# Performance work log

Hardware: AMD Instinct MI355X
Metric: run time of the kernel (lower is better)

Reference implementation:

```python
import jax, jax.numpy as jnp
import numpy as np

S, B, T, H, E, V, OOV = 400, 16, 64, 512, 256, 50000, 50


def _w(k, shape, scale=0.02):
    return scale * jax.random.normal(k, shape, dtype=jnp.float32)


def setup_inputs() -> dict:
    key = jax.random.key(0)
    ks = jax.random.split(key, 20)
    H2 = H // 2
    return {
        "inputs": jax.random.randint(ks[0], (S, B), 0, V),
        "inputs_length": jnp.full((B,), S, dtype=jnp.int32),  # full lengths (packing is then a no-op)
        "inputs_extended": jax.random.randint(ks[1], (S, B), 0, V + OOV),
        "oov_size": OOV,
        "outputs": jax.random.randint(ks[2], (T, B), 0, V),
        "embedding": _w(ks[3], (V, E)),
        "enc_Wih_f": _w(ks[4], (4 * H2, E)), "enc_Whh_f": _w(ks[5], (4 * H2, H2)),
        "enc_bih_f": jnp.zeros(4 * H2), "enc_bhh_f": jnp.zeros(4 * H2),
        "enc_Wih_b": _w(ks[6], (4 * H2, E)), "enc_Whh_b": _w(ks[7], (4 * H2, H2)),
        "enc_bih_b": jnp.zeros(4 * H2), "enc_bhh_b": jnp.zeros(4 * H2),
        "feat_W": _w(ks[8], (H, H)),
        "dec_Wih": _w(ks[9], (4 * H, E)), "dec_Whh": _w(ks[10], (4 * H, H)),
        "dec_bih": jnp.zeros(4 * H), "dec_bhh": jnp.zeros(4 * H),
        "attn_W": _w(ks[11], (H, H)),
        "vocab_W": _w(ks[12], (V, 3 * H)), "vocab_b": jnp.zeros(V),
        "ptr_W": _w(ks[13], (1, 3 * H)), "ptr_b": jnp.zeros(1),
    }


def _lstm(xs, Wih, Whh, bih, bhh, reverse=False):
    # xs: [S, B, E] -> ys [S, B, H2], final (h, c)
    Bn, H2 = xs.shape[1], Whh.shape[1]

    def step(carry, x):
        h, c = carry
        g = x @ Wih.T + bih + h @ Whh.T + bhh
        i, f, gg, o = jnp.split(g, 4, axis=-1)  # pytorch gate order i,f,g,o
        c = jax.nn.sigmoid(f) * c + jax.nn.sigmoid(i) * jnp.tanh(gg)
        h = jax.nn.sigmoid(o) * jnp.tanh(c)
        return (h, c), h

    init = (jnp.zeros((Bn, H2), xs.dtype), jnp.zeros((Bn, H2), xs.dtype))
    (h, c), ys = jax.lax.scan(step, init, xs, reverse=reverse)
    return ys, h, c


def _forward(inputs, inputs_extended, oov_size, outputs, embedding,
             enc_Wih_f, enc_Whh_f, enc_bih_f, enc_bhh_f,
             enc_Wih_b, enc_Whh_b, enc_bih_b, enc_bhh_b,
             feat_W, dec_Wih, dec_Whh, dec_bih, dec_bhh,
             attn_W, vocab_W, vocab_b, ptr_W, ptr_b):
    Hn = dec_Whh.shape[1]
    Tn, Bn = outputs.shape
    Sn = inputs.shape[0]

    x = embedding[inputs]  # [S,B,E]
    yf, hf, cf = _lstm(x, enc_Wih_f, enc_Whh_f, enc_bih_f, enc_bhh_f)
    yb, hb, cb = _lstm(x, enc_Wih_b, enc_Whh_b, enc_bih_b, enc_bhh_b, reverse=True)
    enc_seq = jnp.concatenate([yf, yb], axis=-1)              # [S,B,H]
    enc_out = jnp.transpose(enc_seq @ feat_W.T, (1, 2, 0))    # Permute(1,2,0) -> [B,H,S]
    # View(-1, H) on [2,B,H/2] stacked states (faithful reshape, incl. batch mixing)
    h0 = jnp.stack([hf, hb]).reshape(-1, Hn)                  # [B,H]
    c0 = jnp.stack([cf, cb]).reshape(-1, Hn)

    yemb = embedding[outputs]                                 # [T,B,E]
    idx = inputs_extended.T                                   # [B,S]
    rows = jnp.arange(Bn)[:, None]
    t_ids = jnp.arange(Tn)

    def step(carry, inp):
        t, xt = inp
        h, c, prev_attn, hid_buf = carry
        # LSTMCell
        g = xt @ dec_Wih.T + dec_bih + h @ dec_Whh.T + dec_bhh
        i, f, gg, o = jnp.split(g, 4, axis=-1)
        c = jax.nn.sigmoid(f) * c + jax.nn.sigmoid(i) * jnp.tanh(gg)
        h = jax.nn.sigmoid(o) * jnp.tanh(c)
        # intra-temporal attention (NB: faithful to source, the *normalized*
        # previous attention is fed back as temporal_scores_sum)
        scores = jnp.exp(jnp.einsum('bh,bhs->bs', h, enc_out))   # [B,S]
        attn = jnp.where(t == 0, scores, scores / prev_attn)
        attn = attn / attn.sum(-1, keepdims=True)                # Normalize(-1)
        enc_ctx = jnp.einsum('bs,bhs->bh', attn, enc_out)        # [B,H]
        # intra-decoder attention over previous decoder hiddens
        keys = hid_buf @ attn_W.T                                # [T,B,H]
        sc = jnp.einsum('bh,tbh->bt', h, keys)
        sc = jnp.where(t_ids[None, :] < t, sc, -1e30)
        a = jax.nn.softmax(sc, axis=-1)
        dec_ctx = jnp.where(t == 0, 0.0, jnp.einsum('bt,tbh->bh', a, hid_buf))
        hid_buf = hid_buf.at[t].set(h)
        # pointer-generator
        feats = jnp.concatenate([h, enc_ctx, dec_ctx], axis=-1)  # [B,3H]
        vdist = jax.nn.softmax(feats @ vocab_W.T + vocab_b, axis=1)
        p = jax.nn.sigmoid(feats @ ptr_W.T + ptr_b)              # [B,1]
        vdist = (1.0 - p) * vdist
        copy = p * attn                                          # [B,S]
        vpad = jnp.pad(vdist, ((0, 0), (0, oov_size)))
        final = vpad.at[rows, idx].add(copy)                     # scatter_add
        return (h, c, attn, hid_buf), final

    hid_buf0 = jnp.zeros((Tn, Bn, Hn))
    init = (h0, c0, jnp.ones((Bn, Sn)), hid_buf0)
    _, preds = jax.lax.scan(step, init, (t_ids, yemb))
    return preds  # [T, B, V+oov]


def reference(inputs, inputs_length, inputs_extended, oov_size, outputs, embedding,
              enc_Wih_f, enc_Whh_f, enc_bih_f, enc_bhh_f,
              enc_Wih_b, enc_Whh_b, enc_bih_b, enc_bhh_b,
              feat_W, dec_Wih, dec_Whh, dec_bih, dec_bhh,
              attn_W, vocab_W, vocab_b, ptr_W, ptr_b):
    # inputs_length is full-length here, so packed RNN == plain scan
    return _forward(inputs, inputs_extended, oov_size, outputs, embedding,
                    enc_Wih_f, enc_Whh_f, enc_bih_f, enc_bhh_f,
                    enc_Wih_b, enc_Whh_b, enc_bih_b, enc_bhh_b,
                    feat_W, dec_Wih, dec_Whh, dec_bih, dec_bhh,
                    attn_W, vocab_W, vocab_b, ptr_W, ptr_b)
```

## Files before the change

### kernel.cpp

```cpp
#include <hip/hip_runtime.h>
#include <cstdint>
#include <cstddef>

typedef unsigned char uchar;
typedef unsigned short ushort;
typedef unsigned int uint;
typedef unsigned long long u64;
typedef __attribute__((ext_vector_type(4))) float f32x4;
typedef __attribute__((ext_vector_type(4))) uint u32x4;
typedef __attribute__((ext_vector_type(4))) int i32x4;

#define DI __device__ __forceinline__

#define S_  400
#define B_  16
#define T_  64
#define H_  512
#define H2_ 256
#define E_  256
#define V_  50000
#define VO_ 50050
#define LP_ 50048

constexpr size_t O_WENCWIH  = 0;
constexpr size_t O_WDECWIH  = O_WENCWIH + (size_t)2048*256*2;
constexpr size_t O_WDECWHH  = O_WDECWIH + (size_t)2048*256*2;
constexpr size_t O_WFEAT    = O_WDECWHH + (size_t)2048*512*2;
constexpr size_t O_WATTN    = O_WFEAT   + (size_t)512*512*2;
constexpr size_t O_BENC     = O_WATTN   + (size_t)512*512*2;
constexpr size_t O_BDEC     = O_BENC    + 2048*4;
constexpr size_t O_WENCWHH8 = O_BDEC    + 2048*4;
constexpr size_t O_XENC     = O_WENCWHH8+ (size_t)2*1024*256;
constexpr size_t O_XDEC     = O_XENC    + (size_t)6400*256*2;
constexpr size_t O_XINENC   = O_XDEC    + (size_t)1024*256*2;
constexpr size_t O_XD       = O_XINENC  + (size_t)2*400*16*1024*2;
constexpr size_t O_ENCSEQ   = O_XD      + (size_t)64*16*2048*2;
constexpr size_t O_ENCOUT   = O_ENCSEQ  + (size_t)6400*512*2;
constexpr size_t O_HFIN     = O_ENCOUT  + (size_t)16*400*512*2;
constexpr size_t O_CFIN     = O_HFIN    + 8192*4;
constexpr size_t O_HBUF     = O_CFIN    + 8192*4;
constexpr size_t O_CSTATE   = O_HBUF    + (size_t)2*8192*2;
constexpr size_t O_HIDBUF   = O_CSTATE  + 8192*4;
constexpr size_t O_KEYS     = O_HIDBUF  + (size_t)64*8192*2;
constexpr size_t O_ATTN     = O_KEYS    + (size_t)64*8192*2;
constexpr size_t O_ATTNQ    = O_ATTN    + (size_t)64*16*400*4;
constexpr size_t O_PSUM     = O_ATTNQ   + (size_t)64*16*400*4;
constexpr size_t O_CTXSLOT  = O_PSUM    + 2*32*16*4;
constexpr size_t O_FEATS    = O_CTXSLOT + (size_t)32*16*512*4;
constexpr size_t O_P        = O_FEATS   + (size_t)1024*1536;
constexpr size_t O_INVSUM   = O_P       + 1024*4;
constexpr size_t O_VOCAB8   = O_INVSUM  + 1024*4;
constexpr size_t O_LOGITS   = O_VOCAB8  + (size_t)50048*1536;
constexpr size_t O_A16      = O_XINENC;
constexpr size_t O_ENCT     = O_A16   + (size_t)16*64*416*2;
constexpr size_t O_HIDT     = O_ENCT  + (size_t)16*512*416*2;

DI float b2f(ushort u){ uint x = ((uint)u) << 16; return __builtin_bit_cast(float, x); }
DI ushort f2b(float f){
  uint u = __builtin_bit_cast(uint, f);
  return (ushort)((u + 0x7fffu + ((u >> 16) & 1u)) >> 16);
}
DI uchar f2e4(float f){
  int q = __builtin_amdgcn_cvt_pk_fp8_f32(f, 0.f, 0, false);
  return (uchar)(q & 0xff);
}
DI uchar f2i8(float f, float scale){
  float q = rintf(f * scale);
  q = fminf(127.f, fmaxf(-127.f, q));
  return (uchar)(signed char)(int)q;
}
DI float e42f(uint b){ return __builtin_amdgcn_cvt_f32_fp8((int)b, 0); }
DI float sigm(float x){ return 1.f / (1.f + __expf(-x)); }
DI float tanhf_(float x){ return 2.f / (1.f + __expf(-2.f * x)) - 1.f; }

DI f32x4 mfma16_bf16(u32x4 a, u32x4 b, f32x4 c){
  asm("v_mfma_f32_16x16x32_bf16 %0, %1, %2, %0" : "+v"(c) : "v"(a), "v"(b));
  return c;
}
DI f32x4 mfma16_fp8(u64 a, u64 b, f32x4 c){
  asm("v_mfma_f32_16x16x32_fp8_fp8 %0, %1, %2, %0" : "+v"(c) : "v"(a), "v"(b));
  return c;
}
DI i32x4 mfma16_i8(u32x4 a, u32x4 b, i32x4 c){
  asm("v_mfma_i32_16x16x64_i8 %0, %1, %2, %0" : "+v"(c) : "v"(a), "v"(b));
  return c;
}
DI void mfma_fence(){ asm volatile("s_nop 7\n\ts_nop 7"); }
DI void barrier_lds(){ asm volatile("s_waitcnt lgkmcnt(0)\n\ts_barrier" ::: "memory"); }
DI void wait_vm0(){ asm volatile("s_waitcnt vmcnt(0)" ::: "memory"); }

typedef __attribute__((address_space(1))) const uchar GU;
typedef __attribute__((address_space(3))) uchar LU;
DI void gload16(const uchar* g, uchar* l){
  __builtin_amdgcn_global_load_lds((GU*)g, (LU*)l, 16, 0, 0);
}

DI float fp8exp4(uint w){
  return __expf(__builtin_amdgcn_cvt_f32_fp8((int)w, 0) * (1.f/1024.f))
       + __expf(__builtin_amdgcn_cvt_f32_fp8((int)w, 1) * (1.f/1024.f))
       + __expf(__builtin_amdgcn_cvt_f32_fp8((int)w, 2) * (1.f/1024.f))
       + __expf(__builtin_amdgcn_cvt_f32_fp8((int)w, 3) * (1.f/1024.f));
}

struct X4 { ushort a, b, c, d; };

__global__ void k_prep(const float* __restrict__ eWf, const float* __restrict__ eWb,
                       const float* __restrict__ dW,  const float* __restrict__ dWhh,
                       const float* __restrict__ fW,  const float* __restrict__ aW,
                       const float* __restrict__ eHf, const float* __restrict__ eHb,
                       const float* __restrict__ bif, const float* __restrict__ bhf,
                       const float* __restrict__ bib, const float* __restrict__ bhb,
                       const float* __restrict__ dbi, const float* __restrict__ dbh,
                       ushort* __restrict__ oEW, ushort* __restrict__ oDW,
                       ushort* __restrict__ oDWhh, ushort* __restrict__ oF,
                       ushort* __restrict__ oA, uchar* __restrict__ oH8,
                       float* __restrict__ oBE, float* __restrict__ oBD){
  const int seg = blockIdx.y;
  const int stride = gridDim.x * 256;
  int n = 262144;
  if (seg == 2) n = 524288;
  else if (seg == 3) n = 1048576;
  else if (seg == 8 || seg == 9) n = 1024;
  else if (seg == 10) n = 2048;
  for (int i = blockIdx.x*256 + threadIdx.x; i < n; i += stride) {
    switch (seg) {
      case 0:  oEW[i]        = f2b(eWf[i]); break;
      case 1:  oEW[262144+i] = f2b(eWb[i]); break;
      case 2:  oDW[i]        = f2b(dW[i]);  break;
      case 3:  oDWhh[i]      = f2b(dWhh[i]);break;
      case 4:  oF[i]         = f2b(fW[i]);  break;
      case 5:  oA[i]         = f2b(aW[i]);  break;
      case 6:  oH8[i]        = f2i8(eHf[i], 1024.f); break;
      case 7:  oH8[262144+i] = f2i8(eHb[i], 1024.f); break;
      case 8:  oBE[i]        = bif[i]+bhf[i]; break;
      case 9:  oBE[1024+i]   = bib[i]+bhb[i]; break;
      case 10: oBD[i]        = dbi[i]+dbh[i]; break;
    }
  }
}

__global__ void k_embed(const int* __restrict__ inp, const int* __restrict__ outp,
                        const float* __restrict__ emb,
                        ushort* __restrict__ xenc, ushort* __restrict__ xdec){
  const int total1 = 6400*32, total2 = 1024*32;
  for (int i = blockIdx.x*256 + threadIdx.x; i < total1 + total2; i += gridDim.x*256) {
    const bool enc = i < total1;
    const int jj = enc ? i : i - total1;
    const int row = jj >> 5, e0 = (jj & 31) << 3;
    const int idx = enc ? inp[row] : outp[row];
    const float4* s4 = (const float4*)(emb + ((size_t)idx << 8) + e0);
    float4 v0 = s4[0], v1 = s4[1];
    uint4 o;
    o.x = (uint)f2b(v0.x) | ((uint)f2b(v0.y) << 16);
    o.y = (uint)f2b(v0.z) | ((uint)f2b(v0.w) << 16);
    o.z = (uint)f2b(v1.x) | ((uint)f2b(v1.y) << 16);
    o.w = (uint)f2b(v1.z) | ((uint)f2b(v1.w) << 16);
    *(uint4*)((enc ? xenc : xdec) + ((size_t)row << 8) + e0) = o;
  }
}

template<int ELSZ, int EPI>
__global__ __launch_bounds__(256)
void k_gemm(const uchar* __restrict__ A, const uchar* __restrict__ Bm,
            int mtiles, int kbytes, int arow, int brow,
            uchar* __restrict__ dst, const float* __restrict__ bias){
  __shared__ __align__(16) uchar sm[32768];
  const int tid = threadIdx.x;
  int bx = blockIdx.x;
  if ((gridDim.x & 7) == 0) {
    const int nb = gridDim.x >> 3;
    bx = (bx & 7) * nb + (bx >> 3);
  }
  const int mt = bx % mtiles, nt = bx / mtiles;
  const int m0 = mt << 7, n0 = nt << 7;
  const int w = tid >> 6, l = tid & 63, lr = l & 15, lh = l >> 4;
  const int wr = w >> 1, wc = w & 1;

  f32x4 acc[4][4];
#pragma unroll
  for (int i = 0; i < 4; ++i)
#pragma unroll
    for (int j = 0; j < 4; ++j) { f32x4 z = {0.f,0.f,0.f,0.f}; acc[i][j] = z; }

  const int iters = kbytes >> 6;
  const int roff = tid << 4;
  const int r0 = roff >> 6, c0 = roff & 63;
  const uchar* pa0 = A  + (size_t)(m0 + r0)      * arow + c0;
  const uchar* pa1 = A  + (size_t)(m0 + r0 + 64) * arow + c0;
  const uchar* pb0 = Bm + (size_t)(n0 + r0)      * brow + c0;
  const uchar* pb1 = Bm + (size_t)(n0 + r0 + 64) * brow + c0;

  auto issue = [&](int kt){
    const int ko = kt << 6;
    uchar* db = sm + ((kt & 1) << 14);
    gload16(pa0 + ko, db + roff);
    gload16(pa1 + ko, db + 4096 + roff);
    gload16(pb0 + ko, db + 8192 + roff);
    gload16(pb1 + ko, db + 12288 + roff);
  };

  issue(0);
  wait_vm0();
  __syncthreads();

  for (int kt = 0; kt < iters; ++kt) {
    if (kt + 1 < iters) issue(kt + 1);
    const uchar* smc = sm + ((kt & 1) << 14);
    if constexpr (ELSZ == 2) {
      u32x4 af[4], bf[4];
#pragma unroll
      for (int i = 0; i < 4; ++i) af[i] = *(const u32x4*)(smc + ((wr<<6)+(i<<4)+lr)*64 + (lh<<4));
#pragma unroll
      for (int j = 0; j < 4; ++j) bf[j] = *(const u32x4*)(smc + 8192 + ((wc<<6)+(j<<4)+lr)*64 + (lh<<4));
#pragma unroll
      for (int i = 0; i < 4; ++i)
#pragma unroll
        for (int j = 0; j < 4; ++j) acc[i][j] = mfma16_bf16(af[i], bf[j], acc[i][j]);
    } else {
#pragma unroll
      for (int kk = 0; kk < 2; ++kk) {
        u64 af[4], bf[4];
#pragma unroll
        for (int i = 0; i < 4; ++i) af[i] = *(const u64*)(smc + ((wr<<6)+(i<<4)+lr)*64 + (kk<<5) + (lh<<3));
#pragma unroll
        for (int j = 0; j < 4; ++j) bf[j] = *(const u64*)(smc + 8192 + ((wc<<6)+(j<<4)+lr)*64 + (kk<<5) + (lh<<3));
#pragma unroll
        for (int i = 0; i < 4; ++i)
#pragma unroll
          for (int j = 0; j < 4; ++j) acc[i][j] = mfma16_fp8(af[i], bf[j], acc[i][j]);
      }
    }
    wait_vm0();
    __syncthreads();
  }
  mfma_fence();

  if constexpr (EPI == 0 || EPI == 1) {
#pragma unroll
    for (int j = 0; j < 4; ++j) {
      const int n = n0 + (wc<<6) + (j<<4) + lr;
      const float bz = bias[n];
#pragma unroll
      for (int i = 0; i < 4; ++i)
#pragma unroll
        for (int r = 0; r < 4; ++r) {
          const int m = m0 + (wr<<6) + (i<<4) + (lh<<2) + r;
          const float v = acc[i][j][r] + bz;
          size_t addr;
          if constexpr (EPI == 0) {
            addr = ((size_t)((n >> 10)*6400 + m) << 10) + (n & 1023);
          } else {
            addr = ((size_t)m << 11) + n;
          }
          ((ushort*)dst)[addr] = f2b(v);
        }
    }
  } else if constexpr (EPI == 4) {
#pragma unroll
    for (int j = 0; j < 4; ++j) {
      const int n = n0 + (wc<<6) + (j<<4) + lr;
#pragma unroll
      for (int i = 0; i < 4; ++i)
#pragma unroll
        for (int r = 0; r < 4; ++r) {
          const int m = m0 + (wr<<6)+(i<<4)+(lh<<2)+r;
          ((ushort*)dst)[ ((size_t)m << 9) + n ] = f2b(acc[i][j][r]);
        }
    }
  } else {
    __syncthreads();
#pragma unroll
    for (int j = 0; j < 4; ++j) {
      const int nl = (wc<<6) + (j<<4) + lr;
      const int n = n0 + nl;
      const float bz = (n < V_) ? bias[n] : 0.f;
#pragma unroll
      for (int i = 0; i < 4; ++i)
#pragma unroll
        for (int r = 0; r < 4; ++r) {
          const int ml = (wr<<6)+(i<<4)+(lh<<2)+r;
          const float v = acc[i][j][r] * (1.f/2048.f) + bz;
          sm[ml*128 + nl] = f2e4(v * 1024.f);
        }
    }
    __syncthreads();
    const int row = tid >> 1, half = tid & 1;
    const uchar* srow = sm + row*128 + (half<<6);
    uchar* grow = dst + (size_t)(m0 + row) * LP_ + n0 + (half<<6);
#pragma unroll
    for (int cc4 = 0; cc4 < 4; ++cc4) {
      const int n = n0 + (half<<6) + (cc4<<4);
      if (n + 16 <= V_) {
        *(uint4*)(grow + (cc4<<4)) = *(const uint4*)(srow + (cc4<<4));
      } else {
        for (int bb = 0; bb < 16; ++bb) if (n + bb < V_) grow[(cc4<<4)+bb] = srow[(cc4<<4)+bb];
      }
    }
  }
}

__global__ __launch_bounds__(256)
void k_tr(const ushort* __restrict__ enc, ushort* __restrict__ encT){
  const int bid = blockIdx.x;
  const int b = bid / 20, rem = bid % 20;
  const int sc = rem >> 2, hc = rem & 3;
  const int s0 = sc*80, h0 = hc << 7;
  __shared__ ushort tl[80*130];
  const int t = threadIdx.x;
#pragma unroll
  for (int i = 0; i < 40; ++i) {
    const int idx = t + i*256;
    const int hh = idx & 127, si = idx >> 7;
    tl[si*130 + hh] = enc[ ((size_t)(((s0+si)<<4) + b) << 9) + h0 + hh ];
  }
  __syncthreads();
#pragma unroll
  for (int i = 0; i < 40; ++i) {
    const int idx = t + i*256;
    const int ss = idx % 80, hh = idx / 80;
    encT[ ((size_t)((b<<9) + h0 + hh))*416 + s0 + ss ] = tl[ss*130 + hh];
  }
}

__global__ __launch_bounds__(1024)
void k_encoder(const ushort* __restrict__ Xin, const uchar* __restrict__ Whh8,
               ushort* __restrict__ encseq, float* __restrict__ hfin, float* __restrict__ cfin,
               const float* __restrict__ vocabW, uchar* __restrict__ vocab8){
  const int bid = blockIdx.x;
  const int tid = threadIdx.x;
  if (bid >= 32) {
    const int n4 = 19200000, ntot4 = 19218432;
    const int stride = (gridDim.x - 32) * 1024;
    for (int i = (bid - 32)*1024 + tid; i < ntot4; i += stride) {
      uint o = 0;
      if (i < n4) {
        const float4 v = *(const float4*)(vocabW + (size_t)i*4);
        int lo = __builtin_amdgcn_cvt_pk_fp8_f32(v.x*16.f, v.y*16.f, 0, false);
        int hi = __builtin_amdgcn_cvt_pk_fp8_f32(v.z*16.f, v.w*16.f, 0, false);
        o = ((uint)lo & 0xffffu) | ((uint)hi << 16);
      }
      *(uint*)(vocab8 + (size_t)i*4) = o;
    }
    return;
  }
  const int d = bid >> 4, bglob = bid & 15;
  const int w = tid >> 6, l = tid & 63, lr = l & 15, lh = l >> 4;
  __shared__ __align__(16) uchar hl[2][1024];
  __shared__ float gl[1024];
  for (int i = tid; i < 2048; i += 1024) ((uchar*)hl)[i] = 0;
  u32x4 bfrag[4][4];
  const uchar* Wd = Whh8 + ((size_t)d << 18);
#pragma unroll
  for (int g = 0; g < 4; ++g)
#pragma unroll
    for (int kk = 0; kk < 4; ++kk)
      bfrag[g][kk] = *(const u32x4*)(Wd + (((size_t)((g<<8) + (w<<4) + lr)) << 8) + (kk<<6) + (lh<<4));
  const int base_a = (lr == 0) ? (lh << 4) : 512;
  const int astep  = (lr == 0) ? 64 : 0;
  const int u = tid;
  float cc = 0.f;
  const ushort* xin_base = Xin + ((size_t)(d*6400) << 10);

  auto xld = [&](int s) -> X4 {
    const int t = d ? 399 - s : s;
    const ushort* p = xin_base + (((size_t)(t*16 + bglob)) << 10) + u;
    X4 r; r.a = p[0]; r.b = p[256]; r.c = p[512]; r.d = p[768];
    return r;
  };

  auto STEP = [&](int s, X4 xv) {
    const int cur = s & 1;
    i32x4 z = {0,0,0,0};
    i32x4 a0 = z, a1 = z, a2 = z, a3 = z;
#pragma unroll
    for (int kk = 0; kk < 4; ++kk) {
      const u32x4 a = *(const u32x4*)&hl[cur][base_a + kk*astep];
      a0 = mfma16_i8(a, bfrag[0][kk], a0);
      a1 = mfma16_i8(a, bfrag[1][kk], a1);
      a2 = mfma16_i8(a, bfrag[2][kk], a2);
      a3 = mfma16_i8(a, bfrag[3][kk], a3);
    }
    mfma_fence();
    if (lh == 0) {
      const int uu = (w<<4) + lr;
      gl[uu]       = (float)a0[0];
      gl[256+uu]   = (float)a1[0];
      gl[512+uu]   = (float)a2[0];
      gl[768+uu]   = (float)a3[0];
    }
    barrier_lds();
    if (tid < 256) {
      const int t = d ? 399 - s : s;
      const float gi = b2f(xv.a) + gl[u]      *(1.f/8388608.f);
      const float gf = b2f(xv.b) + gl[256+u]  *(1.f/8388608.f);
      const float gg = b2f(xv.c) + gl[512+u]  *(1.f/8388608.f);
      const float go = b2f(xv.d) + gl[768+u]  *(1.f/8388608.f);
      cc = sigm(gf)*cc + sigm(gi)*tanhf_(gg);
      const float h = sigm(go)*tanhf_(cc);
      encseq[ ((size_t)((t<<4) + bglob) << 9) + (d<<8) + u ] = f2b(h);
      hl[cur^1][u] = f2i8(h, 8192.f);
      if (s == 399) {
        hfin[ (((d<<4)+bglob) << 8) + u ] = h;
        cfin[ (((d<<4)+bglob) << 8) + u ] = cc;
      }
    }
    barrier_lds();
  };

  X4 xv0 = {0,0,0,0};
  if (tid < 256) xv0 = xld(0);
  barrier_lds();
  for (int s = 0; s < 400; s += 2) {
    X4 xv1 = {0,0,0,0};
    if (tid < 256) xv1 = xld(s + 1);
    STEP(s, xv0);
    if (tid < 256) xv0 = xld(s + 2 <= 399 ? s + 2 : 399);
    STEP(s + 1, xv1);
  }
}

__global__ void k_h0z(const float* __restrict__ hfin, const float* __restrict__ cfin,
                      ushort* __restrict__ hbuf, float* __restrict__ cstate,
                      ushort* __restrict__ encT){
  const int tid = blockIdx.x*256 + threadIdx.x;
  if (tid < 8192) {
    const int r = tid >> 9, ch = tid & 511;
    const int d = r >> 3, b = ((r & 7) << 1) + (ch >> 8), u = ch & 255;
    const int src = (((d<<4)+b) << 8) + u;
    hbuf[8192 + tid] = f2b(hfin[src]);
    cstate[tid] = cfin[src];
  }
  if (tid < 16*512*16) {
    const int b = tid >> 13, h = (tid >> 4) & 511, sp = tid & 15;
    encT[((size_t)((b<<9) + h))*416 + 400 + sp] = 0;
  }
}

__global__ __launch_bounds__(256)
void k_lstm(int t, const ushort* __restrict__ Xd, const ushort* __restrict__ Whh,
            ushort* __restrict__ hbuf, float* __restrict__ cstate,
            ushort* __restrict__ hidbuf, ushort* __restrict__ hidT,
            uchar* __restrict__ feats){
  const int q = blockIdx.x, tid = threadIdx.x;
  const int w = tid >> 6, l = tid & 63, lr = l & 15, lh = l >> 4;
  __shared__ float gl[4][16][16];
  const ushort* hprev = hbuf + (((t+1)&1) << 13);
  f32x4 acc = {0.f,0.f,0.f,0.f};
  const ushort* Wrow = Whh + ((size_t)((w<<9) + (q<<4) + lr) << 9);
#pragma unroll
  for (int kk = 0; kk < 16; ++kk) {
    u32x4 a = *(const u32x4*)(hprev + (lr<<9) + (kk<<5) + (lh<<3));
    u32x4 b = *(const u32x4*)(Wrow + (kk<<5) + (lh<<3));
    acc = mfma16_bf16(a, b, acc);
  }
  mfma_fence();
#pragma unroll
  for (int r = 0; r < 4; ++r) {
    const int b = (lh<<2) + r;
    const float xvv = b2f(Xd[ ((size_t)((t<<4)+b) << 11) + (w<<9) + (q<<4) + lr ]);
    gl[w][b][lr] = acc[r] + xvv;
  }
  __syncthreads();
  const int b = tid >> 4, ul = tid & 15, uu = (q<<4) + ul;
  const float gi = gl[0][b][ul], gf = gl[1][b][ul], gg = gl[2][b][ul], go = gl[3][b][ul];
  float cc = cstate[(b<<9) + uu];
  cc = sigm(gf)*cc + sigm(gi)*tanhf_(gg);
  const float h = sigm(go)*tanhf_(cc);
  cstate[(b<<9)+uu] = cc;
  const ushort hb16 = f2b(h);
  hbuf[((t&1)<<13) + (b<<9) + uu] = hb16;
  hidbuf[((size_t)t<<13) + (b<<9) + uu] = hb16;
  hidT[((size_t)((b<<9)+uu) << 6) + t] = hb16;
  feats[(size_t)((t<<4)+b)*1536 + uu] = f2e4(h*128.f);
}

__global__ __launch_bounds__(256)
void k_score(const ushort* __restrict__ hid, const ushort* __restrict__ enc,
             float* __restrict__ E){
  const int b = blockIdx.x / 5, nc = blockIdx.x % 5;
  const int w = threadIdx.x >> 6, l = threadIdx.x & 63, lr = l & 15, lh = l >> 4;
  f32x4 acc[5];
#pragma unroll
  for (int j = 0; j < 5; ++j) { f32x4 z = {0.f,0.f,0.f,0.f}; acc[j] = z; }
#pragma unroll 4
  for (int kk = 0; kk < 16; ++kk) {
    const u32x4 a = *(const u32x4*)(hid + ((size_t)(((w<<4)+lr)<<4 | b) << 9) + (kk<<5) + (lh<<3));
#pragma unroll
    for (int j = 0; j < 5; ++j) {
      const int s = nc*80 + j*16 + lr;
      const u32x4 bb = *(const u32x4*)(enc + ((size_t)((s<<4) + b) << 9) + (kk<<5) + (lh<<3));
      acc[j] = mfma16_bf16(a, bb, acc[j]);
    }
  }
  mfma_fence();
#pragma unroll
  for (int j = 0; j < 5; ++j)
#pragma unroll
    for (int r = 0; r < 4; ++r) {
      const int t = (w<<4) + (lh<<2) + r;
      const int s = nc*80 + j*16 + lr;
      E[ ((size_t)(t*16 + b))*400 + s ] = __expf(acc[j][r]);
    }
}

__global__ __launch_bounds__(256)
void k_tnorm(const float* __restrict__ E, float* __restrict__ attnB,
             ushort* __restrict__ a16){
  const int b = blockIdx.x, tid = threadIdx.x;
  const int s0 = tid, s1 = tid + 256;
  __shared__ float red[4];
  __shared__ float bcv, qsv;
  float qp0 = 1.f, qp1 = 1.f, qsp = 1.f;
  for (int t = 0; t < 64; ++t) {
    const float e0 = E[ ((size_t)(t*16 + b))*400 + s0 ];
    const float e1 = (s1 < 400) ? E[ ((size_t)(t*16 + b))*400 + s1 ] : 0.f;
    const float q0 = t ? e0 * qsp / qp0 : e0;
    const float q1 = (s1 < 400) ? (t ? e1 * qsp / qp1 : e1) : 0.f;
    qp0 = q0; if (s1 < 400) qp1 = q1;
    float ss = q0 + q1;
#pragma unroll
    for (int off = 32; off > 0; off >>= 1) ss += __shfl_down(ss, off, 64);
    if ((tid & 63) == 0) red[tid >> 6] = ss;
    __syncthreads();
    if (tid == 0) {
      const float tot = red[0] + red[1] + red[2] + red[3];
      qsv = tot; bcv = 1.f / tot;
    }
    __syncthreads();
    const float inv = bcv;
    attnB[ ((size_t)(t*16 + b))*400 + s0 ] = q0 * inv;
    a16[ ((size_t)(b*64 + t))*416 + s0 ] = f2b(q0 * inv);
    if (s1 < 416) {
      if (s1 < 400) attnB[ ((size_t)(t*16 + b))*400 + s1 ] = q1 * inv;
      a16[ ((size_t)(b*64 + t))*416 + s1 ] = (s1 < 400) ? f2b(q1 * inv) : (ushort)0;
    }
    qsp = qsv;
    __syncthreads();
  }
}

__global__ __launch_bounds__(256)
void k_ctx(const ushort* __restrict__ a16, const ushort* __restrict__ encT,
           uchar* __restrict__ feats){
  const int b = blockIdx.x;
  const int w = threadIdx.x >> 6, l = threadIdx.x & 63, lr = l & 15, lh = l >> 4;
  f32x4 acc[4][8];
#pragma unroll
  for (int i = 0; i < 4; ++i)
#pragma unroll
    for (int j = 0; j < 8; ++j) { f32x4 z = {0.f,0.f,0.f,0.f}; acc[i][j] = z; }
  for (int kk = 0; kk < 13; ++kk) {
    u32x4 a[4];
#pragma unroll
    for (int mf = 0; mf < 4; ++mf)
      a[mf] = *(const u32x4*)(a16 + ((size_t)(b*64 + (mf<<4)+lr))*416 + (kk<<5) + (lh<<3));
#pragma unroll
    for (int j = 0; j < 8; ++j) {
      const int h = ((w<<3)+j)*16 + lr;
      const u32x4 bb = *(const u32x4*)(encT + ((size_t)((b<<9)+h))*416 + (kk<<5) + (lh<<3));
#pragma unroll
      for (int mf = 0; mf < 4; ++mf) acc[mf][j] = mfma16_bf16(a[mf], bb, acc[mf][j]);
    }
  }
  mfma_fence();
#pragma unroll
  for (int mf = 0; mf < 4; ++mf)
#pragma unroll
    for (int j = 0; j < 8; ++j)
#pragma unroll
      for (int r = 0; r < 4; ++r) {
        const int t = (mf<<4) + (lh<<2) + r;
        const int h = ((w<<3)+j)*16 + lr;
        feats[ (size_t)((t<<4)+b)*1536 + 512 + h ] = f2e4(acc[mf][j][r] * 128.f);
      }
}

__global__ __launch_bounds__(256)
void k_dattn(const ushort* __restrict__ hid, const ushort* __restrict__ keys,
             const ushort* __restrict__ hidT, uchar* __restrict__ feats){
  const int b = blockIdx.x;
  const int tid = threadIdx.x;
  const int w = tid >> 6, l = tid & 63, lr = l & 15, lh = l >> 4;
  __shared__ float sc[64*65];
  __shared__ ushort pb[64*72];
  {
    f32x4 acc[4];
#pragma unroll
    for (int i = 0; i < 4; ++i) { f32x4 z = {0.f,0.f,0.f,0.f}; acc[i] = z; }
#pragma unroll 4
    for (int kk = 0; kk < 16; ++kk) {
      const u32x4 bb = *(const u32x4*)(keys + ((size_t)((((w<<4)+lr)<<4) + b) << 9) + (kk<<5) + (lh<<3));
#pragma unroll
      for (int mf = 0; mf < 4; ++mf) {
        const u32x4 a = *(const u32x4*)(hid + ((size_t)((((mf<<4)+lr)<<4) + b) << 9) + (kk<<5) + (lh<<3));
        acc[mf] = mfma16_bf16(a, bb, acc[mf]);
      }
    }
    mfma_fence();
#pragma unroll
    for (int mf = 0; mf < 4; ++mf)
#pragma unroll
      for (int r = 0; r < 4; ++r)
        sc[ ((mf<<4)+(lh<<2)+r)*65 + (w<<4)+lr ] = acc[mf][r];
  }
  __syncthreads();
  for (int rr = 0; rr < 16; ++rr) {
    const int row = (w<<4) + rr;
    const float v = sc[row*65 + l];
    const bool act = l < row;
    float vm = act ? v : -3.0e38f;
    float m = vm;
#pragma unroll
    for (int off = 32; off > 0; off >>= 1) m = fmaxf(m, __shfl_xor(m, off, 64));
    const float e = act ? __expf(vm - m) : 0.f;
    float ssum = e;
#pragma unroll
    for (int off = 32; off > 0; off >>= 1) ssum += __shfl_xor(ssum, off, 64);
    const float p = (row == 0) ? 0.f : e / ssum;
    pb[row*72 + l] = f2b(p);
  }
  __syncthreads();
  {
    f32x4 acc[4][8];
#pragma unroll
    for (int i = 0; i < 4; ++i)
#pragma unroll
      for (int j = 0; j < 8; ++j) { f32x4 z = {0.f,0.f,0.f,0.f}; acc[i][j] = z; }
#pragma unroll
    for (int kk = 0; kk < 2; ++kk) {
      u32x4 a[4];
#pragma unroll
      for (int mf = 0; mf < 4; ++mf)
        a[mf] = *(const u32x4*)&pb[ ((mf<<4)+lr)*72 + (kk<<5) + (lh<<3) ];
#pragma unroll
      for (int j = 0; j < 8; ++j) {
        const int h = ((w<<3)+j)*16 + lr;
        const u32x4 bb = *(const u32x4*)(hidT + ((size_t)((b<<9)+h) << 6) + (kk<<5) + (lh<<3));
#pragma unroll
        for (int mf = 0; mf < 4; ++mf) acc[mf][j] = mfma16_bf16(a[mf], bb, acc[mf][j]);
      }
    }
    mfma_fence();
#pragma unroll
    for (int mf = 0; mf < 4; ++mf)
#pragma unroll
      for (int j = 0; j < 8; ++j)
#pragma unroll
        for (int r = 0; r < 4; ++r) {
          const int t = (mf<<4) + (lh<<2) + r;
          const int h = ((w<<3)+j)*16 + lr;
          feats[ (size_t)((t<<4)+b)*1536 + 1024 + h ] = f2e4(acc[mf][j][r] * 128.f);
        }
  }
}

__global__ __launch_bounds__(256)
void k_final2(const uchar* __restrict__ logits, const uchar* __restrict__ feats,
              const float* __restrict__ ptrW, const float* __restrict__ ptrb,
              const float* __restrict__ attnB, const int* __restrict__ iext,
              float* __restrict__ out){
  const int row = blockIdx.x, tid = threadIdx.x;
  const uchar* lrow = logits + (size_t)row * LP_;
  float s = 0.f;
  for (int c = tid*16; c < V_; c += 4096) {
    const uint4 v = *(const uint4*)(lrow + c);
    s += fp8exp4(v.x) + fp8exp4(v.y) + fp8exp4(v.z) + fp8exp4(v.w);
  }
  const uchar* f = feats + (size_t)row*1536;
  float pd = 0.f;
  for (int k = tid*4; k < 1536; k += 1024) {
    const uint wv = *(const uint*)(f + k);
    pd += __builtin_amdgcn_cvt_f32_fp8((int)wv,0)*ptrW[k]
        + __builtin_amdgcn_cvt_f32_fp8((int)wv,1)*ptrW[k+1]
        + __builtin_amdgcn_cvt_f32_fp8((int)wv,2)*ptrW[k+2]
        + __builtin_amdgcn_cvt_f32_fp8((int)wv,3)*ptrW[k+3];
  }
#pragma unroll
  for (int off = 32; off > 0; off >>= 1) {
    s  += __shfl_down(s,  off, 64);
    pd += __shfl_down(pd, off, 64);
  }
  __shared__ float wsum[4], wpd[4];
  __shared__ float oms, pvs;
  if ((tid & 63) == 0) { wsum[tid>>6] = s; wpd[tid>>6] = pd; }
  __syncthreads();
  if (tid == 0) {
    const float pv = sigm((wpd[0]+wpd[1]+wpd[2]+wpd[3]) * (1.f/128.f) + ptrb[0]);
    pvs = pv;
    oms = (1.f - pv) / (wsum[0]+wsum[1]+wsum[2]+wsum[3]);
  }
  __syncthreads();
  const float om = oms;
  float* orow = out + (size_t)row * VO_;
  for (int v = tid; v < VO_; v += 256) {
    float val = 0.f;
    if (v < V_) val = om * __expf(e42f((uint)lrow[v]) * (1.f/1024.f));
    orow[v] = val;
  }
  __syncthreads();
  const float pv = pvs;
  const int b = row & 15;
  const float* arow = attnB + (size_t)row*400;
  for (int sidx = tid; sidx < 400; sidx += 256) {
    atomicAdd(orow + iext[sidx*16 + b], pv * arow[sidx]);
  }
}

extern "C" void kernel_launch(void* const* d_in, const int* in_sizes, int n_in,
                              void* d_out, int out_size, void* d_ws, size_t ws_size,
                              hipStream_t stream){
  (void)in_sizes; (void)n_in; (void)out_size; (void)ws_size;
  const int*   inputs     = (const int*)  d_in[0];
  const int*   inputs_ext = (const int*)  d_in[2];
  const int*   outputs    = (const int*)  d_in[4];
  const float* embedding  = (const float*)d_in[5];
  const float* enc_Wih_f  = (const float*)d_in[6];
  const float* enc_Whh_f  = (const float*)d_in[7];
  const float* enc_bih_f  = (const float*)d_in[8];
  const float* enc_bhh_f  = (const float*)d_in[9];
  const float* enc_Wih_b  = (const float*)d_in[10];
  const float* enc_Whh_b  = (const float*)d_in[11];
  const float* enc_bih_b  = (const float*)d_in[12];
  const float* enc_bhh_b  = (const float*)d_in[13];
  const float* feat_W     = (const float*)d_in[14];
  const float* dec_Wih    = (const float*)d_in[15];
  const float* dec_Whh    = (const float*)d_in[16];
  const float* dec_bih    = (const float*)d_in[17];
  const float* dec_bhh    = (const float*)d_in[18];
  const float* attn_W     = (const float*)d_in[19];
  const float* vocab_W    = (const float*)d_in[20];
  const float* vocab_b    = (const float*)d_in[21];
  const float* ptr_W      = (const float*)d_in[22];
  const float* ptr_b      = (const float*)d_in[23];

  uchar* W = (uchar*)d_ws;
  ushort* wEncWih  = (ushort*)(W + O_WENCWIH);
  ushort* wDecWih  = (ushort*)(W + O_WDECWIH);
  ushort* wDecWhh  = (ushort*)(W + O_WDECWHH);
  ushort* wFeat    = (ushort*)(W + O_WFEAT);
  ushort* wAttn    = (ushort*)(W + O_WATTN);
  float*  bEnc     = (float*) (W + O_BENC);
  float*  bDec     = (float*) (W + O_BDEC);
  uchar*  wEncWhh8 = (uchar*) (W + O_WENCWHH8);
  ushort* xEnc     = (ushort*)(W + O_XENC);
  ushort* xDec     = (ushort*)(W + O_XDEC);
  ushort* XinEnc   = (ushort*)(W + O_XINENC);
  ushort* Xd       = (ushort*)(W + O_XD);
  ushort* encSeq   = (ushort*)(W + O_ENCSEQ);
  ushort* encOut   = (ushort*)(W + O_ENCOUT);
  float*  hFin     = (float*) (W + O_HFIN);
  float*  cFin     = (float*) (W + O_CFIN);
  ushort* hBuf     = (ushort*)(W + O_HBUF);
  float*  cState   = (float*) (W + O_CSTATE);
  ushort* hidBuf   = (ushort*)(W + O_HIDBUF);
  ushort* keys     = (ushort*)(W + O_KEYS);
  float*  attnB    = (float*) (W + O_ATTN);
  float*  Ebuf     = (float*) (W + O_ATTNQ);
  ushort* a16      = (ushort*)(W + O_A16);
  ushort* encT     = (ushort*)(W + O_ENCT);
  ushort* hidT     = (ushort*)(W + O_HIDT);
  uchar*  feats    = (uchar*) (W + O_FEATS);
  uchar*  vocab8   = (uchar*) (W + O_VOCAB8);
  uchar*  logits   = (uchar*) (W + O_LOGITS);
  float*  out      = (float*) d_out;

  k_prep<<<dim3(96, 11), 256, 0, stream>>>(enc_Wih_f, enc_Wih_b, dec_Wih, dec_Whh, feat_W, attn_W,
                                           enc_Whh_f, enc_Whh_b, enc_bih_f, enc_bhh_f,
                                           enc_bih_b, enc_bhh_b, dec_bih, dec_bhh,
                                           wEncWih, wDecWih, wDecWhh, wFeat, wAttn,
                                           wEncWhh8, bEnc, bDec);

  k_embed<<<928, 256, 0, stream>>>(inputs, outputs, embedding, xEnc, xDec);

  k_gemm<2,0><<<50*16, 256, 0, stream>>>((const uchar*)xEnc, (const uchar*)wEncWih,
                                         50, 512, 512, 512, (uchar*)XinEnc, bEnc);
  k_gemm<2,1><<<8*16, 256, 0, stream>>>((const uchar*)xDec, (const uchar*)wDecWih,
                                        8, 512, 512, 512, (uchar*)Xd, bDec);

  k_encoder<<<256, 1024, 0, stream>>>(XinEnc, wEncWhh8, encSeq, hFin, cFin, vocab_W, vocab8);
  k_h0z<<<512, 256, 0, stream>>>(hFin, cFin, hBuf, cState, encT);

  k_gemm<2,4><<<50*4, 256, 0, stream>>>((const uchar*)encSeq, (const uchar*)wFeat,
                                        50, 1024, 1024, 1024, (uchar*)encOut, nullptr);
  k_tr<<<320, 256, 0, stream>>>(encOut, encT);

  for (int t = 0; t < T_; ++t) {
    k_lstm<<<32, 256, 0, stream>>>(t, Xd, wDecWhh, hBuf, cState, hidBuf, hidT, feats);
  }

  k_gemm<2,4><<<8*4, 256, 0, stream>>>((const uchar*)hidBuf, (const uchar*)wAttn,
                                       8, 1024, 1024, 1024, (uchar*)keys, nullptr);
  k_score<<<80, 256, 0, stream>>>(hidBuf, encOut, Ebuf);
  k_tnorm<<<16, 256, 0, stream>>>(Ebuf, attnB, a16);
  k_ctx<<<16, 256, 0, stream>>>(a16, encT, feats);
  k_dattn<<<16, 256, 0, stream>>>(hidBuf, keys, hidT, feats);

  k_gemm<1,3><<<8*391, 256, 0, stream>>>(feats, vocab8, 8, 1536, 1536, 1536, logits, vocab_b);

  k_final2<<<1024, 256, 0, stream>>>(logits, feats, ptr_W, ptr_b, attnB, inputs_ext, out);
}
```

Baseline: 1.447 ms.

## Replace int8 MFMA recurrent matvec with per-thread dot4 row products

The encoder LSTM recurrent step, which multiplies a single batch row vector by Whh, no longer uses 16x16x64 int8 MFMA tiles that were mostly padding. Each of the 1024 threads now holds one full 256-byte Whh row in registers and computes its gate pre-activation with v_dot4_i32_i8 over the broadcast int8 hidden state in LDS. This removes the wasted MFMA work, the MFMA dependency fence and the lane-selective writes on the serial per-timestep critical path. In exchange it uses 64 VGPRs per thread for the weight row and issues 64 dot instructions per step.

```diff
diff --git a/kernel.cpp b/kernel.cpp
--- a/kernel.cpp
+++ b/kernel.cpp
@@ -81,13 +81,19 @@
   asm("v_mfma_f32_16x16x32_fp8_fp8 %0, %1, %2, %0" : "+v"(c) : "v"(a), "v"(b));
   return c;
 }
-DI i32x4 mfma16_i8(u32x4 a, u32x4 b, i32x4 c){
-  asm("v_mfma_i32_16x16x64_i8 %0, %1, %2, %0" : "+v"(c) : "v"(a), "v"(b));
-  return c;
-}
 DI void mfma_fence(){ asm volatile("s_nop 7\n\ts_nop 7"); }
 DI void barrier_lds(){ asm volatile("s_waitcnt lgkmcnt(0)\n\ts_barrier" ::: "memory"); }
 DI void wait_vm0(){ asm volatile("s_waitcnt vmcnt(0)" ::: "memory"); }
+
+DI int dot4(int a, int b, int c){
+#if __has_builtin(__builtin_amdgcn_sdot4)
+  return __builtin_amdgcn_sdot4(a, b, c, false);
+#else
+  int d;
+  asm("v_dot4_i32_i8 %0, %1, %2, %3" : "=v"(d) : "v"(a), "v"(b), "v"(c));
+  return d;
+#endif
+}
 
 typedef __attribute__((address_space(1))) const uchar GU;
 typedef __attribute__((address_space(3))) uchar LU;
@@ -344,20 +350,14 @@
     return;
   }
   const int d = bid >> 4, bglob = bid & 15;
-  const int w = tid >> 6, l = tid & 63, lr = l & 15, lh = l >> 4;
-  __shared__ __align__(16) uchar hl[2][1024];
+  __shared__ __align__(16) uchar hl[2][256];
   __shared__ float gl[1024];
-  for (int i = tid; i < 2048; i += 1024) ((uchar*)hl)[i] = 0;
-  u32x4 bfrag[4][4];
-  const uchar* Wd = Whh8 + ((size_t)d << 18);
-#pragma unroll
-  for (int g = 0; g < 4; ++g)
-#pragma unroll
-    for (int kk = 0; kk < 4; ++kk)
-      bfrag[g][kk] = *(const u32x4*)(Wd + (((size_t)((g<<8) + (w<<4) + lr)) << 8) + (kk<<6) + (lh<<4));
-  const int base_a = (lr == 0) ? (lh << 4) : 512;
-  const int astep  = (lr == 0) ? 64 : 0;
-  const int u = tid;
+  if (tid < 128) ((uint*)hl)[tid] = 0;
+  u32x4 wf[16];
+  const uchar* Wr = Whh8 + ((size_t)d << 18) + ((size_t)tid << 8);
+#pragma unroll
+  for (int j = 0; j < 16; ++j) wf[j] = *(const u32x4*)(Wr + (j << 4));
+  const int u = tid & 255;
   float cc = 0.f;
   const ushort* xin_base = Xin + ((size_t)(d*6400) << 10);
 
@@ -370,24 +370,17 @@
 
   auto STEP = [&](int s, X4 xv) {
     const int cur = s & 1;
-    i32x4 z = {0,0,0,0};
-    i32x4 a0 = z, a1 = z, a2 = z, a3 = z;
-#pragma unroll
-    for (int kk = 0; kk < 4; ++kk) {
-      const u32x4 a = *(const u32x4*)&hl[cur][base_a + kk*astep];
-      a0 = mfma16_i8(a, bfrag[0][kk], a0);
-      a1 = mfma16_i8(a, bfrag[1][kk], a1);
-      a2 = mfma16_i8(a, bfrag[2][kk], a2);
-      a3 = mfma16_i8(a, bfrag[3][kk], a3);
-    }
-    mfma_fence();
-    if (lh == 0) {
-      const int uu = (w<<4) + lr;
-      gl[uu]       = (float)a0[0];
-      gl[256+uu]   = (float)a1[0];
-      gl[512+uu]   = (float)a2[0];
-      gl[768+uu]   = (float)a3[0];
-    }
+    const u32x4* hp = (const u32x4*)&hl[cur][0];
+    int a0 = 0, a1 = 0, a2 = 0, a3 = 0;
+#pragma unroll
+    for (int j = 0; j < 16; ++j) {
+      const u32x4 h4 = hp[j];
+      a0 = dot4((int)h4[0], (int)wf[j][0], a0);
+      a1 = dot4((int)h4[1], (int)wf[j][1], a1);
+      a2 = dot4((int)h4[2], (int)wf[j][2], a2);
+      a3 = dot4((int)h4[3], (int)wf[j][3], a3);
+    }
+    gl[tid] = (float)((a0 + a1) + (a2 + a3));
     barrier_lds();
     if (tid < 256) {
       const int t = d ? 399 - s : s;
```

After: 1.469 ms. Within noise of the previous version (+1.5%).
